# Kernel tuning notes

Measured on AMD Instinct MI355X. Metric: run time of the kernel, lower is better.

## Reference

```python
import jax, jax.numpy as jnp
import numpy as np

TOP_K = 2


def setup_inputs() -> dict:
    key = jax.random.key(0)
    k_x, k_g, k_w1, k_w2, k_w3 = jax.random.split(key, 5)
    B, S, D, H, E = 2, 512, 1024, 512, 8
    x = jax.random.normal(k_x, (B, S, D), dtype=jnp.float32)
    gate_w = jax.random.normal(k_g, (D, E), dtype=jnp.float32) * (D ** -0.5)
    w1 = jax.random.normal(k_w1, (E, D, H), dtype=jnp.float32) * 0.02  # gate proj
    w2 = jax.random.normal(k_w2, (E, H, D), dtype=jnp.float32) * 0.02  # down proj
    w3 = jax.random.normal(k_w3, (E, D, H), dtype=jnp.float32) * 0.02  # up proj
    return {"x": x, "gate_w": gate_w, "w1": w1, "w2": w2, "w3": w3}


def reference(x, gate_w, w1, w2, w3):
    # Token-choice top-k MoE with grouped SwiGLU experts, no shared expert.
    # Equivalent to torchtune MoE: gather routed tokens, scale by top-k router
    # score, run per-expert FFN, scatter-add back. Since each expert's FFN has
    # no bias (FFN(0) == 0), the dispatch/grouped-GEMM/combine is expressed
    # densely as sum_e FFN_e(scale[:, e] * x), which is mathematically identical.
    B, S, D = x.shape
    E = gate_w.shape[1]
    xf = x.reshape(B * S, D)                      # [T, D]
    T = B * S

    logits = xf @ gate_w                          # [T, E]
    scores = jax.nn.softmax(logits, axis=-1)
    top_scores, top_idx = jax.lax.top_k(scores, TOP_K)  # [T, k]

    # scale[t, e] = router score if expert e selected for token t, else 0
    scale = jnp.zeros((T, E), dtype=x.dtype).at[
        jnp.arange(T)[:, None], top_idx
    ].set(top_scores)

    xs = scale.T[:, :, None] * xf[None, :, :]     # [E, T, D] scaled routed input
    h = jax.nn.silu(jnp.einsum('etd,edh->eth', xs, w1)) \
        * jnp.einsum('etd,edh->eth', xs, w3)      # [E, T, H]
    y = jnp.einsum('eth,ehd->etd', h, w2)         # [E, T, D]
    out = y.sum(axis=0)                           # combine (scatter-add equiv)
    return out.reshape(B, S, D)
```

## Files before the change

### kernel.cpp

```cpp
#include <hip/hip_runtime.h>
#include <hip/hip_bf16.h>
#include <cstddef>

#define T_TOK 1024
#define D_DIM 1024
#define H_DIM 512
#define E_EXP 8
#define P_CAP 2560
#define MAX_MT 40
#define LDA 72
#define NK1 16
#define NK2 8

typedef __attribute__((ext_vector_type(4)))  float    float4_t;
typedef __attribute__((ext_vector_type(16))) float    f32x16;
typedef __attribute__((ext_vector_type(8)))  short    short8_t;
typedef __attribute__((ext_vector_type(4)))  unsigned uint4_t;
typedef __attribute__((ext_vector_type(2)))  unsigned uint2_t;

__device__ __forceinline__ short f2bf(float f) {
  union { float f; unsigned u; } v; v.f = f;
  unsigned u = v.u;
  u += 0x7FFFu + ((u >> 16) & 1u);
  return (short)(u >> 16);
}

__device__ __forceinline__ unsigned pkbf(float a, float b) {
  union { __hip_bfloat162 h; unsigned u; } v;
  v.h = __float22bfloat162_rn(make_float2(a, b));
  return v.u;
}

__global__ __launch_bounds__(256) void prep_kernel(
    const float* __restrict__ w1, const float* __restrict__ w3,
    const float* __restrict__ w2, const float* __restrict__ x,
    const float* __restrict__ gw, short* __restrict__ w13t,
    short* __restrict__ w2t, int* __restrict__ idx2,
    float* __restrict__ scale2, float* __restrict__ out) {
  __shared__ float tile[64][69];
  const int z = blockIdx.z;
  const int tid = threadIdx.x;

  if (z < 24) {
    const float* src; short* dst; int N, ldd, row_off;
    if (z < 16) {
      if (blockIdx.y >= 8) return;
      int which = z >> 3, e = z & 7;
      src = (which ? w3 : w1) + (size_t)e * D_DIM * H_DIM;
      dst = w13t + (size_t)e * D_DIM * (2 * H_DIM);
      N = H_DIM; ldd = D_DIM; row_off = which ? H_DIM : 0;
    } else {
      if (blockIdx.x >= 8) return;
      int e = z - 16;
      src = w2 + (size_t)e * H_DIM * D_DIM;
      dst = w2t + (size_t)e * D_DIM * H_DIM;
      N = D_DIM; ldd = H_DIM; row_off = 0;
    }
    const int k0 = blockIdx.x * 64, n0 = blockIdx.y * 64;
    const int kr = tid >> 4, nc = (tid & 15) * 4;
    #pragma unroll
    for (int p = 0; p < 4; ++p) {
      int k = p * 16 + kr;
      float4_t v = *(const float4_t*)(src + (size_t)(k0 + k) * N + n0 + nc);
      tile[k][nc]     = v[0];
      tile[k][nc + 1] = v[1];
      tile[k][nc + 2] = v[2];
      tile[k][nc + 3] = v[3];
    }
    __syncthreads();
    const int r8 = tid >> 3, c8 = tid & 7;
    #pragma unroll
    for (int p = 0; p < 2; ++p) {
      int row = p * 32 + r8;
      uint4_t u;
      #pragma unroll
      for (int jj = 0; jj < 4; ++jj)
        u[jj] = pkbf(tile[c8 * 8 + 2 * jj][row], tile[c8 * 8 + 2 * jj + 1][row]);
      *(uint4_t*)(dst + (size_t)(row_off + n0 + row) * ldd + k0 + c8 * 8) = u;
    }
    return;
  }

  if (z == 25) {
    float4_t z4 = {0.f, 0.f, 0.f, 0.f};
    float4_t* o = (float4_t*)(out + ((size_t)(blockIdx.y * 16 + blockIdx.x)) * 4096);
    #pragma unroll
    for (int i = 0; i < 4; ++i) o[i * 256 + tid] = z4;
    return;
  }

  const int wid  = tid >> 6;
  const int lane = tid & 63;
  const int t = (blockIdx.y * 16 + blockIdx.x) * 4 + wid;
  const float* xr = x + (size_t)t * D_DIM;
  float acc[E_EXP];
  #pragma unroll
  for (int e = 0; e < E_EXP; ++e) acc[e] = 0.f;
  for (int d = lane; d < D_DIM; d += 64) {
    float xv = xr[d];
    float4_t g0 = *(const float4_t*)(gw + d * E_EXP);
    float4_t g1 = *(const float4_t*)(gw + d * E_EXP + 4);
    acc[0] += xv * g0[0]; acc[1] += xv * g0[1];
    acc[2] += xv * g0[2]; acc[3] += xv * g0[3];
    acc[4] += xv * g1[0]; acc[5] += xv * g1[1];
    acc[6] += xv * g1[2]; acc[7] += xv * g1[3];
  }
  #pragma unroll
  for (int off = 32; off >= 1; off >>= 1) {
    #pragma unroll
    for (int e = 0; e < E_EXP; ++e) acc[e] += __shfl_down(acc[e], off, 64);
  }
  if (lane == 0) {
    float m = acc[0];
    #pragma unroll
    for (int e = 1; e < E_EXP; ++e) m = fmaxf(m, acc[e]);
    float p[E_EXP]; float s = 0.f;
    #pragma unroll
    for (int e = 0; e < E_EXP; ++e) { p[e] = __expf(acc[e] - m); s += p[e]; }
    float inv = 1.f / s;
    #pragma unroll
    for (int e = 0; e < E_EXP; ++e) p[e] *= inv;
    int i1 = 0;
    #pragma unroll
    for (int e = 1; e < E_EXP; ++e) if (p[e] > p[i1]) i1 = e;
    int i2 = (i1 == 0) ? 1 : 0;
    #pragma unroll
    for (int e = 0; e < E_EXP; ++e) {
      if (e == i1 || e == i2) continue;
      if (p[e] > p[i2]) i2 = e;
    }
    idx2[2 * t]     = i1;  scale2[2 * t]     = p[i1];
    idx2[2 * t + 1] = i2;  scale2[2 * t + 1] = p[i2];
  }
}

__global__ __launch_bounds__(256) void scan_kernel(
    const int* __restrict__ idx2, const float* __restrict__ scale2,
    int* __restrict__ pair_tok, float* __restrict__ pair_scale,
    int* __restrict__ meta) {
  __shared__ int cnt[E_EXP], base[E_EXP], cur[E_EXP];
  const int tid = threadIdx.x;
  if (tid < E_EXP) { cnt[tid] = 0; cur[tid] = 0; }
  for (int p = tid; p < P_CAP; p += 256) { pair_tok[p] = -1; pair_scale[p] = 0.f; }
  __syncthreads();
  for (int t = tid; t < T_TOK; t += 256) {
    atomicAdd(&cnt[idx2[2 * t]], 1);
    atomicAdd(&cnt[idx2[2 * t + 1]], 1);
  }
  __syncthreads();
  if (tid == 0) {
    int b = 0, g = 0;
    for (int e = 0; e < E_EXP; ++e) {
      base[e] = b;
      int al = (cnt[e] + 63) & ~63;
      for (int j = 0; j < al; j += 64) { meta[1 + g] = e; meta[81 + g] = b + j; ++g; }
      b += al;
    }
    meta[0] = g;
  }
  __syncthreads();
  for (int t = tid; t < T_TOK; t += 256) {
    #pragma unroll
    for (int s = 0; s < 2; ++s) {
      int e = idx2[2 * t + s];
      int p = base[e] + atomicAdd(&cur[e], 1);
      pair_tok[p] = t;
      pair_scale[p] = scale2[2 * t + s];
    }
  }
}

__global__ __launch_bounds__(256) void astage_kernel(
    const float* __restrict__ x, const int* __restrict__ pair_tok,
    const float* __restrict__ pair_scale, short* __restrict__ Ag) {
  const int tid = threadIdx.x;
  const int row = blockIdx.x * 8 + (tid >> 5);
  const int c0  = (tid & 31) * 4;
  const int   tok = pair_tok[row];
  const float sc  = pair_scale[row];
  const float* xr = x + (size_t)(tok < 0 ? 0 : tok) * D_DIM;
  short* orow = Ag + (size_t)row * D_DIM;
  #pragma unroll
  for (int j = 0; j < 8; ++j) {
    int c = c0 + j * 128;
    float4_t v = *(const float4_t*)(xr + c);
    uint2_t u = { pkbf(v[0] * sc, v[1] * sc), pkbf(v[2] * sc, v[3] * sc) };
    *(uint2_t*)(orow + c) = u;
  }
}

__global__ __launch_bounds__(256, 2) void gemm1_kernel(
    const short* __restrict__ Ag, const short* __restrict__ w13t,
    const int* __restrict__ meta, short* __restrict__ h) {
  __shared__ short As[2][64 * LDA];
  __shared__ short B1s[2][64 * LDA];
  __shared__ short B3s[2][64 * LDA];
  const int mt = blockIdx.y;
  if (mt >= meta[0]) return;
  const int e    = meta[1 + mt];
  const int row0 = meta[81 + mt];
  const int n0   = blockIdx.x * 64;
  const int tid = threadIdx.x, lane = tid & 63, wid = tid >> 6;
  const int wm = wid >> 1, wn = wid & 1;
  const int l31 = lane & 31, lh = lane >> 5;
  const short* bsrc = w13t + (size_t)e * D_DIM * (2 * H_DIM);

  const int sr = tid >> 3, su = (tid & 7) * 8;
  const size_t st32 = (size_t)32 * D_DIM;
  const short* apA = Ag   + (size_t)(row0 + sr) * D_DIM + su;
  const short* ap1 = bsrc + (size_t)(n0 + sr) * D_DIM + su;
  const short* ap3 = bsrc + (size_t)(H_DIM + n0 + sr) * D_DIM + su;

  f32x16 acc1, acc3;
  #pragma unroll
  for (int i = 0; i < 16; ++i) { acc1[i] = 0.f; acc3[i] = 0.f; }

  {
    uint4_t a0 = *(const uint4_t*)apA;
    uint4_t a1 = *(const uint4_t*)(apA + st32);
    uint4_t p0 = *(const uint4_t*)ap1;
    uint4_t p1 = *(const uint4_t*)(ap1 + st32);
    uint4_t q0 = *(const uint4_t*)ap3;
    uint4_t q1 = *(const uint4_t*)(ap3 + st32);
    *(uint4_t*)&As[0][sr * LDA + su]         = a0;
    *(uint4_t*)&As[0][(sr + 32) * LDA + su]  = a1;
    *(uint4_t*)&B1s[0][sr * LDA + su]        = p0;
    *(uint4_t*)&B1s[0][(sr + 32) * LDA + su] = p1;
    *(uint4_t*)&B3s[0][sr * LDA + su]        = q0;
    *(uint4_t*)&B3s[0][(sr + 32) * LDA + su] = q1;
  }

  for (int t = 0; t < NK1 - 1; ++t) {
    __syncthreads();
    const int cur = t & 1, nxt = cur ^ 1;
    const int ko = (t + 1) * 64;
    uint4_t a0 = *(const uint4_t*)(apA + ko);
    uint4_t a1 = *(const uint4_t*)(apA + st32 + ko);
    uint4_t p0 = *(const uint4_t*)(ap1 + ko);
    uint4_t p1 = *(const uint4_t*)(ap1 + st32 + ko);
    uint4_t q0 = *(const uint4_t*)(ap3 + ko);
    uint4_t q1 = *(const uint4_t*)(ap3 + st32 + ko);

    short8_t af[4], b1f[4], b3f[4];
    #pragma unroll
    for (int s = 0; s < 4; ++s) {
      const int kof = s * 16 + lh * 8;
      af[s]  = *(const short8_t*)&As[cur][(wm * 32 + l31) * LDA + kof];
      b1f[s] = *(const short8_t*)&B1s[cur][(wn * 32 + l31) * LDA + kof];
      b3f[s] = *(const short8_t*)&B3s[cur][(wn * 32 + l31) * LDA + kof];
    }
    #pragma unroll
    for (int s = 0; s < 4; ++s) {
      acc1 = __builtin_amdgcn_mfma_f32_32x32x16_bf16(af[s], b1f[s], acc1, 0, 0, 0);
      acc3 = __builtin_amdgcn_mfma_f32_32x32x16_bf16(af[s], b3f[s], acc3, 0, 0, 0);
    }
    *(uint4_t*)&As[nxt][sr * LDA + su]         = a0;
    *(uint4_t*)&As[nxt][(sr + 32) * LDA + su]  = a1;
    *(uint4_t*)&B1s[nxt][sr * LDA + su]        = p0;
    *(uint4_t*)&B1s[nxt][(sr + 32) * LDA + su] = p1;
    *(uint4_t*)&B3s[nxt][sr * LDA + su]        = q0;
    *(uint4_t*)&B3s[nxt][(sr + 32) * LDA + su] = q1;
  }
  __syncthreads();
  {
    short8_t af[4], b1f[4], b3f[4];
    #pragma unroll
    for (int s = 0; s < 4; ++s) {
      const int kof = s * 16 + lh * 8;
      af[s]  = *(const short8_t*)&As[1][(wm * 32 + l31) * LDA + kof];
      b1f[s] = *(const short8_t*)&B1s[1][(wn * 32 + l31) * LDA + kof];
      b3f[s] = *(const short8_t*)&B3s[1][(wn * 32 + l31) * LDA + kof];
    }
    #pragma unroll
    for (int s = 0; s < 4; ++s) {
      acc1 = __builtin_amdgcn_mfma_f32_32x32x16_bf16(af[s], b1f[s], acc1, 0, 0, 0);
      acc3 = __builtin_amdgcn_mfma_f32_32x32x16_bf16(af[s], b3f[s], acc3, 0, 0, 0);
    }
  }

  {
    const int col = n0 + wn * 32 + l31;
    #pragma unroll
    for (int r = 0; r < 16; ++r) {
      int mrow = (r & 3) + 8 * (r >> 2) + 4 * lh;
      int grow = row0 + wm * 32 + mrow;
      float c1 = acc1[r], c3 = acc3[r];
      float sig = 1.f / (1.f + __expf(-c1));
      h[(size_t)grow * H_DIM + col] = f2bf(c1 * sig * c3);
    }
  }
}

__global__ __launch_bounds__(256, 2) void gemm2_kernel(
    const short* __restrict__ h, const short* __restrict__ w2t,
    const int* __restrict__ pair_tok, const int* __restrict__ meta,
    float* __restrict__ out) {
  __shared__ short As[2][64 * LDA];
  __shared__ short Bs[2][128 * LDA];
  const int mt = blockIdx.y;
  if (mt >= meta[0]) return;
  const int e    = meta[1 + mt];
  const int row0 = meta[81 + mt];
  const int n0   = blockIdx.x * 128;
  const int tid = threadIdx.x, lane = tid & 63, wid = tid >> 6;
  const int wm = wid >> 1, wn = wid & 1;
  const int l31 = lane & 31, lh = lane >> 5;
  const short* bsrc = w2t + (size_t)e * D_DIM * H_DIM;

  const int sr = tid >> 3, su = (tid & 7) * 8;
  const size_t st32 = (size_t)32 * H_DIM;
  const short* apA = h    + (size_t)(row0 + sr) * H_DIM + su;
  const short* apB = bsrc + (size_t)(n0 + sr) * H_DIM + su;

  f32x16 acc[2];
  #pragma unroll
  for (int i = 0; i < 16; ++i) { acc[0][i] = 0.f; acc[1][i] = 0.f; }

  {
    uint4_t a0 = *(const uint4_t*)apA;
    uint4_t a1 = *(const uint4_t*)(apA + st32);
    uint4_t b0 = *(const uint4_t*)apB;
    uint4_t b1 = *(const uint4_t*)(apB + st32);
    uint4_t b2 = *(const uint4_t*)(apB + 2 * st32);
    uint4_t b3 = *(const uint4_t*)(apB + 3 * st32);
    *(uint4_t*)&As[0][sr * LDA + su]         = a0;
    *(uint4_t*)&As[0][(sr + 32) * LDA + su]  = a1;
    *(uint4_t*)&Bs[0][sr * LDA + su]         = b0;
    *(uint4_t*)&Bs[0][(sr + 32) * LDA + su]  = b1;
    *(uint4_t*)&Bs[0][(sr + 64) * LDA + su]  = b2;
    *(uint4_t*)&Bs[0][(sr + 96) * LDA + su]  = b3;
  }

  for (int t = 0; t < NK2 - 1; ++t) {
    __syncthreads();
    const int cur = t & 1, nxt = cur ^ 1;
    const int ko = (t + 1) * 64;
    uint4_t a0 = *(const uint4_t*)(apA + ko);
    uint4_t a1 = *(const uint4_t*)(apA + st32 + ko);
    uint4_t b0 = *(const uint4_t*)(apB + ko);
    uint4_t b1 = *(const uint4_t*)(apB + st32 + ko);
    uint4_t b2 = *(const uint4_t*)(apB + 2 * st32 + ko);
    uint4_t b3 = *(const uint4_t*)(apB + 3 * st32 + ko);

    short8_t af[4], bf[2][4];
    #pragma unroll
    for (int s = 0; s < 4; ++s) {
      const int kof = s * 16 + lh * 8;
      af[s] = *(const short8_t*)&As[cur][(wm * 32 + l31) * LDA + kof];
      #pragma unroll
      for (int j = 0; j < 2; ++j)
        bf[j][s] = *(const short8_t*)&Bs[cur][(wn * 64 + j * 32 + l31) * LDA + kof];
    }
    #pragma unroll
    for (int s = 0; s < 4; ++s) {
      acc[0] = __builtin_amdgcn_mfma_f32_32x32x16_bf16(af[s], bf[0][s], acc[0], 0, 0, 0);
      acc[1] = __builtin_amdgcn_mfma_f32_32x32x16_bf16(af[s], bf[1][s], acc[1], 0, 0, 0);
    }
    *(uint4_t*)&As[nxt][sr * LDA + su]         = a0;
    *(uint4_t*)&As[nxt][(sr + 32) * LDA + su]  = a1;
    *(uint4_t*)&Bs[nxt][sr * LDA + su]         = b0;
    *(uint4_t*)&Bs[nxt][(sr + 32) * LDA + su]  = b1;
    *(uint4_t*)&Bs[nxt][(sr + 64) * LDA + su]  = b2;
    *(uint4_t*)&Bs[nxt][(sr + 96) * LDA + su]  = b3;
  }
  __syncthreads();
  {
    short8_t af[4], bf[2][4];
    #pragma unroll
    for (int s = 0; s < 4; ++s) {
      const int kof = s * 16 + lh * 8;
      af[s] = *(const short8_t*)&As[1][(wm * 32 + l31) * LDA + kof];
      #pragma unroll
      for (int j = 0; j < 2; ++j)
        bf[j][s] = *(const short8_t*)&Bs[1][(wn * 64 + j * 32 + l31) * LDA + kof];
    }
    #pragma unroll
    for (int s = 0; s < 4; ++s) {
      acc[0] = __builtin_amdgcn_mfma_f32_32x32x16_bf16(af[s], bf[0][s], acc[0], 0, 0, 0);
      acc[1] = __builtin_amdgcn_mfma_f32_32x32x16_bf16(af[s], bf[1][s], acc[1], 0, 0, 0);
    }
  }

  {
    #pragma unroll
    for (int r = 0; r < 16; ++r) {
      int mrow = (r & 3) + 8 * (r >> 2) + 4 * lh;
      int grow = row0 + wm * 32 + mrow;
      int tok = pair_tok[grow];
      if (tok < 0) continue;
      float* orow = out + (size_t)tok * D_DIM;
      #pragma unroll
      for (int j = 0; j < 2; ++j) {
        int col = n0 + wn * 64 + j * 32 + l31;
        atomicAdd(orow + col, acc[j][r]);
      }
    }
  }
}

extern "C" void kernel_launch(void* const* d_in, const int* in_sizes, int n_in,
                              void* d_out, int out_size, void* d_ws, size_t ws_size,
                              hipStream_t stream) {
  const float* x  = (const float*)d_in[0];
  const float* gw = (const float*)d_in[1];
  const float* w1 = (const float*)d_in[2];
  const float* w2 = (const float*)d_in[3];
  const float* w3 = (const float*)d_in[4];
  float* out = (float*)d_out;

  char* ws = (char*)d_ws;
  int*   idx2    = (int*)  (ws);
  float* scale2  = (float*)(ws + 8192);
  int*   ptok    = (int*)  (ws + 16384);
  float* pscale  = (float*)(ws + 32768);
  int*   meta    = (int*)  (ws + 49152);
  short* h       = (short*)(ws + (1u << 20));
  short* w13t    = (short*)(ws + (4u << 20));
  short* w2t     = (short*)(ws + (21u << 20));
  short* Ag      = (short*)(ws + (30u << 20));

  prep_kernel<<<dim3(16, 16, 26), dim3(256), 0, stream>>>(
      w1, w3, w2, x, gw, w13t, w2t, idx2, scale2, out);
  scan_kernel<<<dim3(1), dim3(256), 0, stream>>>(idx2, scale2, ptok, pscale, meta);
  astage_kernel<<<dim3(P_CAP / 8), dim3(256), 0, stream>>>(x, ptok, pscale, Ag);
  gemm1_kernel<<<dim3(H_DIM / 64, MAX_MT), dim3(256), 0, stream>>>(
      Ag, w13t, meta, h);
  gemm2_kernel<<<dim3(D_DIM / 128, MAX_MT), dim3(256), 0, stream>>>(
      h, w2t, ptok, meta, out);
}
```

Before: 148.5 us.

## Fuse MoE pipeline into one persistent cooperative kernel with grid syncs

Replaces five separate launches (prep/transpose, scan, A staging, gemm1, gemm2) with a single cooperative persistent kernel of 512 blocks. The blocks loop over work units and separate the stages with grid.sync(). The aim is to remove launch gaps and tail idle time between the small stages. The cost is grid-wide barriers, a single-block scan phase while every other block waits, and fixed-grid scheduling of the GEMM tiles. The old multi-kernel path is kept as a fallback if the cooperative launch fails.

Result: slower. 393.2 us (+164.9%).

```diff
diff --git a/kernel.cpp b/kernel.cpp
--- a/kernel.cpp
+++ b/kernel.cpp
@@ -1,6 +1,9 @@
 #include <hip/hip_runtime.h>
+#include <hip/hip_cooperative_groups.h>
 #include <hip/hip_bf16.h>
 #include <cstddef>
+
+namespace cg = cooperative_groups;
 
 #define T_TOK 1024
 #define D_DIM 1024
@@ -11,6 +14,7 @@
 #define LDA 72
 #define NK1 16
 #define NK2 8
+#define GRID_B 512
 
 typedef __attribute__((ext_vector_type(4)))  float    float4_t;
 typedef __attribute__((ext_vector_type(16))) float    f32x16;
@@ -29,6 +33,364 @@
   union { __hip_bfloat162 h; unsigned u; } v;
   v.h = __float22bfloat162_rn(make_float2(a, b));
   return v.u;
+}
+
+union SharedU {
+  float tt[64 * 69];
+  struct { short A[2][64 * LDA], B1[2][64 * LDA], B3[2][64 * LDA]; } g1;
+  struct { short A[2][64 * LDA], B[2][128 * LDA]; } g2;
+};
+
+__device__ __forceinline__ void transpose_tile(
+    const float* __restrict__ src, short* __restrict__ dst, int N, int ldd,
+    int row_off, int k0, int n0, int tid, float* tt) {
+  const int kr = tid >> 4, nc = (tid & 15) * 4;
+  #pragma unroll
+  for (int p = 0; p < 4; ++p) {
+    int k = p * 16 + kr;
+    float4_t v = *(const float4_t*)(src + (size_t)(k0 + k) * N + n0 + nc);
+    tt[k * 69 + nc]     = v[0];
+    tt[k * 69 + nc + 1] = v[1];
+    tt[k * 69 + nc + 2] = v[2];
+    tt[k * 69 + nc + 3] = v[3];
+  }
+  __syncthreads();
+  const int r8 = tid >> 3, c8 = tid & 7;
+  #pragma unroll
+  for (int p = 0; p < 2; ++p) {
+    int row = p * 32 + r8;
+    uint4_t u;
+    #pragma unroll
+    for (int jj = 0; jj < 4; ++jj)
+      u[jj] = pkbf(tt[(c8 * 8 + 2 * jj) * 69 + row], tt[(c8 * 8 + 2 * jj + 1) * 69 + row]);
+    *(uint4_t*)(dst + (size_t)(row_off + n0 + row) * ldd + k0 + c8 * 8) = u;
+  }
+  __syncthreads();
+}
+
+__device__ __forceinline__ void router4(
+    int u, const float* __restrict__ x, const float* __restrict__ gw,
+    int* __restrict__ idx2, float* __restrict__ scale2, int tid) {
+  const int wid = tid >> 6, lane = tid & 63;
+  const int t = u * 4 + wid;
+  const float* xr = x + (size_t)t * D_DIM;
+  float acc[E_EXP];
+  #pragma unroll
+  for (int e = 0; e < E_EXP; ++e) acc[e] = 0.f;
+  for (int d = lane; d < D_DIM; d += 64) {
+    float xv = xr[d];
+    float4_t g0 = *(const float4_t*)(gw + d * E_EXP);
+    float4_t g1 = *(const float4_t*)(gw + d * E_EXP + 4);
+    acc[0] += xv * g0[0]; acc[1] += xv * g0[1];
+    acc[2] += xv * g0[2]; acc[3] += xv * g0[3];
+    acc[4] += xv * g1[0]; acc[5] += xv * g1[1];
+    acc[6] += xv * g1[2]; acc[7] += xv * g1[3];
+  }
+  #pragma unroll
+  for (int off = 32; off >= 1; off >>= 1) {
+    #pragma unroll
+    for (int e = 0; e < E_EXP; ++e) acc[e] += __shfl_down(acc[e], off, 64);
+  }
+  if (lane == 0) {
+    float m = acc[0];
+    #pragma unroll
+    for (int e = 1; e < E_EXP; ++e) m = fmaxf(m, acc[e]);
+    float p[E_EXP]; float s = 0.f;
+    #pragma unroll
+    for (int e = 0; e < E_EXP; ++e) { p[e] = __expf(acc[e] - m); s += p[e]; }
+    float inv = 1.f / s;
+    #pragma unroll
+    for (int e = 0; e < E_EXP; ++e) p[e] *= inv;
+    int i1 = 0;
+    #pragma unroll
+    for (int e = 1; e < E_EXP; ++e) if (p[e] > p[i1]) i1 = e;
+    int i2 = (i1 == 0) ? 1 : 0;
+    #pragma unroll
+    for (int e = 0; e < E_EXP; ++e) {
+      if (e == i1 || e == i2) continue;
+      if (p[e] > p[i2]) i2 = e;
+    }
+    idx2[2 * t]     = i1;  scale2[2 * t]     = p[i1];
+    idx2[2 * t + 1] = i2;  scale2[2 * t + 1] = p[i2];
+  }
+}
+
+__global__ __launch_bounds__(256, 2) void moe_fused(
+    const float* __restrict__ x, const float* __restrict__ gw,
+    const float* __restrict__ w1, const float* __restrict__ w2,
+    const float* __restrict__ w3, short* __restrict__ w13t,
+    short* __restrict__ w2t, int* __restrict__ idx2,
+    float* __restrict__ scale2, int* __restrict__ ptok,
+    float* __restrict__ pscale, int* __restrict__ meta,
+    short* __restrict__ Ag, short* __restrict__ h,
+    float* __restrict__ out) {
+  cg::grid_group grid = cg::this_grid();
+  __shared__ SharedU sh;
+  __shared__ int s_cnt[E_EXP], s_base[E_EXP], s_cur[E_EXP];
+  const int tid = threadIdx.x;
+  const int bid = blockIdx.x;
+
+  for (int u = bid; u < 3594; u += GRID_B) {
+    if (u < 2048) {
+      int z = u >> 7, rem = u & 127;
+      int kt = rem & 15, nt = rem >> 4;
+      int which = z >> 3, e = z & 7;
+      const float* src = (which ? w3 : w1) + (size_t)e * D_DIM * H_DIM;
+      short* dst = w13t + (size_t)e * D_DIM * (2 * H_DIM);
+      transpose_tile(src, dst, H_DIM, D_DIM, which ? H_DIM : 0,
+                     kt * 64, nt * 64, tid, sh.tt);
+    } else if (u < 3072) {
+      int v = u - 2048;
+      int e = v >> 7, rem = v & 127;
+      int kt = rem & 7, nt = rem >> 3;
+      const float* src = w2 + (size_t)e * H_DIM * D_DIM;
+      short* dst = w2t + (size_t)e * D_DIM * H_DIM;
+      transpose_tile(src, dst, D_DIM, H_DIM, 0, kt * 64, nt * 64, tid, sh.tt);
+    } else if (u < 3328) {
+      router4(u - 3072, x, gw, idx2, scale2, tid);
+    } else if (u < 3584) {
+      int v = u - 3328;
+      float4_t z4 = {0.f, 0.f, 0.f, 0.f};
+      float4_t* o = (float4_t*)(out + (size_t)v * 4096);
+      #pragma unroll
+      for (int i = 0; i < 4; ++i) o[i * 256 + tid] = z4;
+    } else {
+      int p = (u - 3584) * 256 + tid;
+      if (p < P_CAP) { ptok[p] = -1; pscale[p] = 0.f; }
+    }
+  }
+  grid.sync();
+
+  if (bid == 0) {
+    if (tid < E_EXP) { s_cnt[tid] = 0; s_cur[tid] = 0; }
+    __syncthreads();
+    for (int t = tid; t < T_TOK; t += 256) {
+      atomicAdd(&s_cnt[idx2[2 * t]], 1);
+      atomicAdd(&s_cnt[idx2[2 * t + 1]], 1);
+    }
+    __syncthreads();
+    if (tid == 0) {
+      int b = 0, g = 0;
+      for (int e = 0; e < E_EXP; ++e) {
+        s_base[e] = b;
+        int al = (s_cnt[e] + 63) & ~63;
+        for (int j = 0; j < al; j += 64) { meta[1 + g] = e; meta[81 + g] = b + j; ++g; }
+        b += al;
+      }
+      meta[0] = g;
+    }
+    __syncthreads();
+    for (int t = tid; t < T_TOK; t += 256) {
+      #pragma unroll
+      for (int s = 0; s < 2; ++s) {
+        int e = idx2[2 * t + s];
+        int p = s_base[e] + atomicAdd(&s_cur[e], 1);
+        ptok[p] = t;
+        pscale[p] = scale2[2 * t + s];
+      }
+    }
+  }
+  grid.sync();
+
+  for (int u = bid; u < P_CAP / 8; u += GRID_B) {
+    const int row = u * 8 + (tid >> 5);
+    const int c0  = (tid & 31) * 4;
+    const int   tok = ptok[row];
+    const float sc  = pscale[row];
+    const float* xr = x + (size_t)(tok < 0 ? 0 : tok) * D_DIM;
+    short* orow = Ag + (size_t)row * D_DIM;
+    #pragma unroll
+    for (int j = 0; j < 8; ++j) {
+      int c = c0 + j * 128;
+      float4_t v = *(const float4_t*)(xr + c);
+      uint2_t uu = { pkbf(v[0] * sc, v[1] * sc), pkbf(v[2] * sc, v[3] * sc) };
+      *(uint2_t*)(orow + c) = uu;
+    }
+  }
+  const int nmt = meta[0];
+  grid.sync();
+
+  const int lane = tid & 63, wid = tid >> 6;
+  const int wm = wid >> 1, wn = wid & 1;
+  const int l31 = lane & 31, lh = lane >> 5;
+  const int sr = tid >> 3, su = (tid & 7) * 8;
+
+  for (int u = bid; u < 8 * nmt; u += GRID_B) {
+    const int nt = u & 7, mt = u >> 3;
+    const int e = meta[1 + mt], row0 = meta[81 + mt];
+    const int n0 = nt * 64;
+    const short* bsrc = w13t + (size_t)e * D_DIM * (2 * H_DIM);
+    const size_t st32 = (size_t)32 * D_DIM;
+    const short* apA = Ag   + (size_t)(row0 + sr) * D_DIM + su;
+    const short* ap1 = bsrc + (size_t)(n0 + sr) * D_DIM + su;
+    const short* ap3 = bsrc + (size_t)(H_DIM + n0 + sr) * D_DIM + su;
+
+    f32x16 acc1, acc3;
+    #pragma unroll
+    for (int i = 0; i < 16; ++i) { acc1[i] = 0.f; acc3[i] = 0.f; }
+
+    {
+      uint4_t a0 = *(const uint4_t*)apA;
+      uint4_t a1 = *(const uint4_t*)(apA + st32);
+      uint4_t p0 = *(const uint4_t*)ap1;
+      uint4_t p1 = *(const uint4_t*)(ap1 + st32);
+      uint4_t q0 = *(const uint4_t*)ap3;
+      uint4_t q1 = *(const uint4_t*)(ap3 + st32);
+      *(uint4_t*)&sh.g1.A[0][sr * LDA + su]         = a0;
+      *(uint4_t*)&sh.g1.A[0][(sr + 32) * LDA + su]  = a1;
+      *(uint4_t*)&sh.g1.B1[0][sr * LDA + su]        = p0;
+      *(uint4_t*)&sh.g1.B1[0][(sr + 32) * LDA + su] = p1;
+      *(uint4_t*)&sh.g1.B3[0][sr * LDA + su]        = q0;
+      *(uint4_t*)&sh.g1.B3[0][(sr + 32) * LDA + su] = q1;
+    }
+    for (int t = 0; t < NK1 - 1; ++t) {
+      __syncthreads();
+      const int cur = t & 1, nxt = cur ^ 1;
+      const int ko = (t + 1) * 64;
+      uint4_t a0 = *(const uint4_t*)(apA + ko);
+      uint4_t a1 = *(const uint4_t*)(apA + st32 + ko);
+      uint4_t p0 = *(const uint4_t*)(ap1 + ko);
+      uint4_t p1 = *(const uint4_t*)(ap1 + st32 + ko);
+      uint4_t q0 = *(const uint4_t*)(ap3 + ko);
+      uint4_t q1 = *(const uint4_t*)(ap3 + st32 + ko);
+      short8_t af[4], b1f[4], b3f[4];
+      #pragma unroll
+      for (int s = 0; s < 4; ++s) {
+        const int kof = s * 16 + lh * 8;
+        af[s]  = *(const short8_t*)&sh.g1.A[cur][(wm * 32 + l31) * LDA + kof];
+        b1f[s] = *(const short8_t*)&sh.g1.B1[cur][(wn * 32 + l31) * LDA + kof];
+        b3f[s] = *(const short8_t*)&sh.g1.B3[cur][(wn * 32 + l31) * LDA + kof];
+      }
+      #pragma unroll
+      for (int s = 0; s < 4; ++s) {
+        acc1 = __builtin_amdgcn_mfma_f32_32x32x16_bf16(af[s], b1f[s], acc1, 0, 0, 0);
+        acc3 = __builtin_amdgcn_mfma_f32_32x32x16_bf16(af[s], b3f[s], acc3, 0, 0, 0);
+      }
+      *(uint4_t*)&sh.g1.A[nxt][sr * LDA + su]         = a0;
+      *(uint4_t*)&sh.g1.A[nxt][(sr + 32) * LDA + su]  = a1;
+      *(uint4_t*)&sh.g1.B1[nxt][sr * LDA + su]        = p0;
+      *(uint4_t*)&sh.g1.B1[nxt][(sr + 32) * LDA + su] = p1;
+      *(uint4_t*)&sh.g1.B3[nxt][sr * LDA + su]        = q0;
+      *(uint4_t*)&sh.g1.B3[nxt][(sr + 32) * LDA + su] = q1;
+    }
+    __syncthreads();
+    {
+      short8_t af[4], b1f[4], b3f[4];
+      #pragma unroll
+      for (int s = 0; s < 4; ++s) {
+        const int kof = s * 16 + lh * 8;
+        af[s]  = *(const short8_t*)&sh.g1.A[1][(wm * 32 + l31) * LDA + kof];
+        b1f[s] = *(const short8_t*)&sh.g1.B1[1][(wn * 32 + l31) * LDA + kof];
+        b3f[s] = *(const short8_t*)&sh.g1.B3[1][(wn * 32 + l31) * LDA + kof];
+      }
+      #pragma unroll
+      for (int s = 0; s < 4; ++s) {
+        acc1 = __builtin_amdgcn_mfma_f32_32x32x16_bf16(af[s], b1f[s], acc1, 0, 0, 0);
+        acc3 = __builtin_amdgcn_mfma_f32_32x32x16_bf16(af[s], b3f[s], acc3, 0, 0, 0);
+      }
+    }
+    __syncthreads();
+    {
+      const int col = n0 + wn * 32 + l31;
+      #pragma unroll
+      for (int r = 0; r < 16; ++r) {
+        int mrow = (r & 3) + 8 * (r >> 2) + 4 * lh;
+        int grow = row0 + wm * 32 + mrow;
+        float c1 = acc1[r], c3 = acc3[r];
+        float sig = 1.f / (1.f + __expf(-c1));
+        h[(size_t)grow * H_DIM + col] = f2bf(c1 * sig * c3);
+      }
+    }
+  }
+  grid.sync();
+
+  for (int u = bid; u < 8 * nmt; u += GRID_B) {
+    const int nt = u & 7, mt = u >> 3;
+    const int e = meta[1 + mt], row0 = meta[81 + mt];
+    const int n0 = nt * 128;
+    const short* bsrc = w2t + (size_t)e * D_DIM * H_DIM;
+    const size_t st32 = (size_t)32 * H_DIM;
+    const short* apA = h    + (size_t)(row0 + sr) * H_DIM + su;
+    const short* apB = bsrc + (size_t)(n0 + sr) * H_DIM + su;
+
+    f32x16 accA, accB;
+    #pragma unroll
+    for (int i = 0; i < 16; ++i) { accA[i] = 0.f; accB[i] = 0.f; }
+
+    {
+      uint4_t a0 = *(const uint4_t*)apA;
+      uint4_t a1 = *(const uint4_t*)(apA + st32);
+      uint4_t b0 = *(const uint4_t*)apB;
+      uint4_t b1 = *(const uint4_t*)(apB + st32);
+      uint4_t b2 = *(const uint4_t*)(apB + 2 * st32);
+      uint4_t b3 = *(const uint4_t*)(apB + 3 * st32);
+      *(uint4_t*)&sh.g2.A[0][sr * LDA + su]        = a0;
+      *(uint4_t*)&sh.g2.A[0][(sr + 32) * LDA + su] = a1;
+      *(uint4_t*)&sh.g2.B[0][sr * LDA + su]        = b0;
+      *(uint4_t*)&sh.g2.B[0][(sr + 32) * LDA + su] = b1;
+      *(uint4_t*)&sh.g2.B[0][(sr + 64) * LDA + su] = b2;
+      *(uint4_t*)&sh.g2.B[0][(sr + 96) * LDA + su] = b3;
+    }
+    for (int t = 0; t < NK2 - 1; ++t) {
+      __syncthreads();
+      const int cur = t & 1, nxt = cur ^ 1;
+      const int ko = (t + 1) * 64;
+      uint4_t a0 = *(const uint4_t*)(apA + ko);
+      uint4_t a1 = *(const uint4_t*)(apA + st32 + ko);
+      uint4_t b0 = *(const uint4_t*)(apB + ko);
+      uint4_t b1 = *(const uint4_t*)(apB + st32 + ko);
+      uint4_t b2 = *(const uint4_t*)(apB + 2 * st32 + ko);
+      uint4_t b3 = *(const uint4_t*)(apB + 3 * st32 + ko);
+      short8_t af[4], bf0[4], bf1[4];
+      #pragma unroll
+      for (int s = 0; s < 4; ++s) {
+        const int kof = s * 16 + lh * 8;
+        af[s]  = *(const short8_t*)&sh.g2.A[cur][(wm * 32 + l31) * LDA + kof];
+        bf0[s] = *(const short8_t*)&sh.g2.B[cur][(wn * 64 + l31) * LDA + kof];
+        bf1[s] = *(const short8_t*)&sh.g2.B[cur][(wn * 64 + 32 + l31) * LDA + kof];
+      }
+      #pragma unroll
+      for (int s = 0; s < 4; ++s) {
+        accA = __builtin_amdgcn_mfma_f32_32x32x16_bf16(af[s], bf0[s], accA, 0, 0, 0);
+        accB = __builtin_amdgcn_mfma_f32_32x32x16_bf16(af[s], bf1[s], accB, 0, 0, 0);
+      }
+      *(uint4_t*)&sh.g2.A[nxt][sr * LDA + su]        = a0;
+      *(uint4_t*)&sh.g2.A[nxt][(sr + 32) * LDA + su] = a1;
+      *(uint4_t*)&sh.g2.B[nxt][sr * LDA + su]        = b0;
+      *(uint4_t*)&sh.g2.B[nxt][(sr + 32) * LDA + su] = b1;
+      *(uint4_t*)&sh.g2.B[nxt][(sr + 64) * LDA + su] = b2;
+      *(uint4_t*)&sh.g2.B[nxt][(sr + 96) * LDA + su] = b3;
+    }
+    __syncthreads();
+    {
+      short8_t af[4], bf0[4], bf1[4];
+      #pragma unroll
+      for (int s = 0; s < 4; ++s) {
+        const int kof = s * 16 + lh * 8;
+        af[s]  = *(const short8_t*)&sh.g2.A[1][(wm * 32 + l31) * LDA + kof];
+        bf0[s] = *(const short8_t*)&sh.g2.B[1][(wn * 64 + l31) * LDA + kof];
+        bf1[s] = *(const short8_t*)&sh.g2.B[1][(wn * 64 + 32 + l31) * LDA + kof];
+      }
+      #pragma unroll
+      for (int s = 0; s < 4; ++s) {
+        accA = __builtin_amdgcn_mfma_f32_32x32x16_bf16(af[s], bf0[s], accA, 0, 0, 0);
+        accB = __builtin_amdgcn_mfma_f32_32x32x16_bf16(af[s], bf1[s], accB, 0, 0, 0);
+      }
+    }
+    __syncthreads();
+    {
+      #pragma unroll
+      for (int r = 0; r < 16; ++r) {
+        int mrow = (r & 3) + 8 * (r >> 2) + 4 * lh;
+        int grow = row0 + wm * 32 + mrow;
+        int tok = ptok[grow];
+        if (tok < 0) continue;
+        float* orow = out + (size_t)tok * D_DIM;
+        atomicAdd(orow + n0 + wn * 64 + l31, accA[r]);
+        atomicAdd(orow + n0 + wn * 64 + 32 + l31, accB[r]);
+      }
+    }
+  }
 }
 
 __global__ __launch_bounds__(256) void prep_kernel(
@@ -37,12 +399,11 @@
     const float* __restrict__ gw, short* __restrict__ w13t,
     short* __restrict__ w2t, int* __restrict__ idx2,
     float* __restrict__ scale2, float* __restrict__ out) {
-  __shared__ float tile[64][69];
+  __shared__ float tile[64 * 69];
   const int z = blockIdx.z;
   const int tid = threadIdx.x;
-
   if (z < 24) {
-    const float* src; short* dst; int N, ldd, row_off;
+    const float* src; short* dst; int N, ldd, row_off, k0, n0;
     if (z < 16) {
       if (blockIdx.y >= 8) return;
       int which = z >> 3, e = z & 7;
@@ -56,31 +417,10 @@
       dst = w2t + (size_t)e * D_DIM * H_DIM;
       N = D_DIM; ldd = H_DIM; row_off = 0;
     }
-    const int k0 = blockIdx.x * 64, n0 = blockIdx.y * 64;
-    const int kr = tid >> 4, nc = (tid & 15) * 4;
-    #pragma unroll
-    for (int p = 0; p < 4; ++p) {
-      int k = p * 16 + kr;
-      float4_t v = *(const float4_t*)(src + (size_t)(k0 + k) * N + n0 + nc);
-      tile[k][nc]     = v[0];
-      tile[k][nc + 1] = v[1];
-      tile[k][nc + 2] = v[2];
-      tile[k][nc + 3] = v[3];
-    }
-    __syncthreads();
-    const int r8 = tid >> 3, c8 = tid & 7;
-    #pragma unroll
-    for (int p = 0; p < 2; ++p) {
-      int row = p * 32 + r8;
-      uint4_t u;
-      #pragma unroll
-      for (int jj = 0; jj < 4; ++jj)
-        u[jj] = pkbf(tile[c8 * 8 + 2 * jj][row], tile[c8 * 8 + 2 * jj + 1][row]);
-      *(uint4_t*)(dst + (size_t)(row_off + n0 + row) * ldd + k0 + c8 * 8) = u;
-    }
+    k0 = blockIdx.x * 64; n0 = blockIdx.y * 64;
+    transpose_tile(src, dst, N, ldd, row_off, k0, n0, tid, tile);
     return;
   }
-
   if (z == 25) {
     float4_t z4 = {0.f, 0.f, 0.f, 0.f};
     float4_t* o = (float4_t*)(out + ((size_t)(blockIdx.y * 16 + blockIdx.x)) * 4096);
@@ -88,50 +428,7 @@
     for (int i = 0; i < 4; ++i) o[i * 256 + tid] = z4;
     return;
   }
-
-  const int wid  = tid >> 6;
-  const int lane = tid & 63;
-  const int t = (blockIdx.y * 16 + blockIdx.x) * 4 + wid;
-  const float* xr = x + (size_t)t * D_DIM;
-  float acc[E_EXP];
-  #pragma unroll
-  for (int e = 0; e < E_EXP; ++e) acc[e] = 0.f;
-  for (int d = lane; d < D_DIM; d += 64) {
-    float xv = xr[d];
-    float4_t g0 = *(const float4_t*)(gw + d * E_EXP);
-    float4_t g1 = *(const float4_t*)(gw + d * E_EXP + 4);
-    acc[0] += xv * g0[0]; acc[1] += xv * g0[1];
-    acc[2] += xv * g0[2]; acc[3] += xv * g0[3];
-    acc[4] += xv * g1[0]; acc[5] += xv * g1[1];
-    acc[6] += xv * g1[2]; acc[7] += xv * g1[3];
-  }
-  #pragma unroll
-  for (int off = 32; off >= 1; off >>= 1) {
-    #pragma unroll
-    for (int e = 0; e < E_EXP; ++e) acc[e] += __shfl_down(acc[e], off, 64);
-  }
-  if (lane == 0) {
-    float m = acc[0];
-    #pragma unroll
-    for (int e = 1; e < E_EXP; ++e) m = fmaxf(m, acc[e]);
-    float p[E_EXP]; float s = 0.f;
-    #pragma unroll
-    for (int e = 0; e < E_EXP; ++e) { p[e] = __expf(acc[e] - m); s += p[e]; }
-    float inv = 1.f / s;
-    #pragma unroll
-    for (int e = 0; e < E_EXP; ++e) p[e] *= inv;
-    int i1 = 0;
-    #pragma unroll
-    for (int e = 1; e < E_EXP; ++e) if (p[e] > p[i1]) i1 = e;
-    int i2 = (i1 == 0) ? 1 : 0;
-    #pragma unroll
-    for (int e = 0; e < E_EXP; ++e) {
-      if (e == i1 || e == i2) continue;
-      if (p[e] > p[i2]) i2 = e;
-    }
-    idx2[2 * t]     = i1;  scale2[2 * t]     = p[i1];
-    idx2[2 * t + 1] = i2;  scale2[2 * t + 1] = p[i2];
-  }
+  router4(blockIdx.y * 16 + blockIdx.x, x, gw, idx2, scale2, tid);
 }
 
 __global__ __launch_bounds__(256) void scan_kernel(
@@ -192,44 +489,31 @@
 __global__ __launch_bounds__(256, 2) void gemm1_kernel(
     const short* __restrict__ Ag, const short* __restrict__ w13t,
     const int* __restrict__ meta, short* __restrict__ h) {
-  __shared__ short As[2][64 * LDA];
-  __shared__ short B1s[2][64 * LDA];
-  __shared__ short B3s[2][64 * LDA];
+  __shared__ SharedU sh;
   const int mt = blockIdx.y;
   if (mt >= meta[0]) return;
-  const int e    = meta[1 + mt];
-  const int row0 = meta[81 + mt];
-  const int n0   = blockIdx.x * 64;
+  const int e = meta[1 + mt], row0 = meta[81 + mt];
+  const int n0 = blockIdx.x * 64;
   const int tid = threadIdx.x, lane = tid & 63, wid = tid >> 6;
   const int wm = wid >> 1, wn = wid & 1;
   const int l31 = lane & 31, lh = lane >> 5;
+  const int sr = tid >> 3, su = (tid & 7) * 8;
   const short* bsrc = w13t + (size_t)e * D_DIM * (2 * H_DIM);
-
-  const int sr = tid >> 3, su = (tid & 7) * 8;
   const size_t st32 = (size_t)32 * D_DIM;
   const short* apA = Ag   + (size_t)(row0 + sr) * D_DIM + su;
   const short* ap1 = bsrc + (size_t)(n0 + sr) * D_DIM + su;
   const short* ap3 = bsrc + (size_t)(H_DIM + n0 + sr) * D_DIM + su;
-
   f32x16 acc1, acc3;
   #pragma unroll
   for (int i = 0; i < 16; ++i) { acc1[i] = 0.f; acc3[i] = 0.f; }
-
   {
-    uint4_t a0 = *(const uint4_t*)apA;
-    uint4_t a1 = *(const uint4_t*)(apA + st32);
-    uint4_t p0 = *(const uint4_t*)ap1;
-    uint4_t p1 = *(const uint4_t*)(ap1 + st32);
-    uint4_t q0 = *(const uint4_t*)ap3;
-    uint4_t q1 = *(const uint4_t*)(ap3 + st32);
-    *(uint4_t*)&As[0][sr * LDA + su]         = a0;
-    *(uint4_t*)&As[0][(sr + 32) * LDA + su]  = a1;
-    *(uint4_t*)&B1s[0][sr * LDA + su]        = p0;
-    *(uint4_t*)&B1s[0][(sr + 32) * LDA + su] = p1;
-    *(uint4_t*)&B3s[0][sr * LDA + su]        = q0;
-    *(uint4_t*)&B3s[0][(sr + 32) * LDA + su] = q1;
-  }
-
+    *(uint4_t*)&sh.g1.A[0][sr * LDA + su]         = *(const uint4_t*)apA;
+    *(uint4_t*)&sh.g1.A[0][(sr + 32) * LDA + su]  = *(const uint4_t*)(apA + st32);
+    *(uint4_t*)&sh.g1.B1[0][sr * LDA + su]        = *(const uint4_t*)ap1;
+    *(uint4_t*)&sh.g1.B1[0][(sr + 32) * LDA + su] = *(const uint4_t*)(ap1 + st32);
+    *(uint4_t*)&sh.g1.B3[0][sr * LDA + su]        = *(const uint4_t*)ap3;
+    *(uint4_t*)&sh.g1.B3[0][(sr + 32) * LDA + su] = *(const uint4_t*)(ap3 + st32);
+  }
   for (int t = 0; t < NK1 - 1; ++t) {
     __syncthreads();
     const int cur = t & 1, nxt = cur ^ 1;
@@ -240,26 +524,25 @@
     uint4_t p1 = *(const uint4_t*)(ap1 + st32 + ko);
     uint4_t q0 = *(const uint4_t*)(ap3 + ko);
     uint4_t q1 = *(const uint4_t*)(ap3 + st32 + ko);
-
     short8_t af[4], b1f[4], b3f[4];
     #pragma unroll
     for (int s = 0; s < 4; ++s) {
       const int kof = s * 16 + lh * 8;
-      af[s]  = *(const short8_t*)&As[cur][(wm * 32 + l31) * LDA + kof];
-      b1f[s] = *(const short8_t*)&B1s[cur][(wn * 32 + l31) * LDA + kof];
-      b3f[s] = *(const short8_t*)&B3s[cur][(wn * 32 + l31) * LDA + kof];
+      af[s]  = *(const short8_t*)&sh.g1.A[cur][(wm * 32 + l31) * LDA + kof];
+      b1f[s] = *(const short8_t*)&sh.g1.B1[cur][(wn * 32 + l31) * LDA + kof];
+      b3f[s] = *(const short8_t*)&sh.g1.B3[cur][(wn * 32 + l31) * LDA + kof];
     }
     #pragma unroll
     for (int s = 0; s < 4; ++s) {
       acc1 = __builtin_amdgcn_mfma_f32_32x32x16_bf16(af[s], b1f[s], acc1, 0, 0, 0);
       acc3 = __builtin_amdgcn_mfma_f32_32x32x16_bf16(af[s], b3f[s], acc3, 0, 0, 0);
     }
-    *(uint4_t*)&As[nxt][sr * LDA + su]         = a0;
-    *(uint4_t*)&As[nxt][(sr + 32) * LDA + su]  = a1;
-    *(uint4_t*)&B1s[nxt][sr * LDA + su]        = p0;
-    *(uint4_t*)&B1s[nxt][(sr + 32) * LDA + su] = p1;
-    *(uint4_t*)&B3s[nxt][sr * LDA + su]        = q0;
-    *(uint4_t*)&B3s[nxt][(sr + 32) * LDA + su] = q1;
+    *(uint4_t*)&sh.g1.A[nxt][sr * LDA + su]         = a0;
+    *(uint4_t*)&sh.g1.A[nxt][(sr + 32) * LDA + su]  = a1;
+    *(uint4_t*)&sh.g1.B1[nxt][sr * LDA + su]        = p0;
+    *(uint4_t*)&sh.g1.B1[nxt][(sr + 32) * LDA + su] = p1;
+    *(uint4_t*)&sh.g1.B3[nxt][sr * LDA + su]        = q0;
+    *(uint4_t*)&sh.g1.B3[nxt][(sr + 32) * LDA + su] = q1;
   }
   __syncthreads();
   {
@@ -267,9 +550,9 @@
     #pragma unroll
     for (int s = 0; s < 4; ++s) {
       const int kof = s * 16 + lh * 8;
-      af[s]  = *(const short8_t*)&As[1][(wm * 32 + l31) * LDA + kof];
-      b1f[s] = *(const short8_t*)&B1s[1][(wn * 32 + l31) * LDA + kof];
-      b3f[s] = *(const short8_t*)&B3s[1][(wn * 32 + l31) * LDA + kof];
+      af[s]  = *(const short8_t*)&sh.g1.A[1][(wm * 32 + l31) * LDA + kof];
+      b1f[s] = *(const short8_t*)&sh.g1.B1[1][(wn * 32 + l31) * LDA + kof];
+      b3f[s] = *(const short8_t*)&sh.g1.B3[1][(wn * 32 + l31) * LDA + kof];
     }
     #pragma unroll
     for (int s = 0; s < 4; ++s) {
@@ -277,7 +560,6 @@
       acc3 = __builtin_amdgcn_mfma_f32_32x32x16_bf16(af[s], b3f[s], acc3, 0, 0, 0);
     }
   }
-
   {
     const int col = n0 + wn * 32 + l31;
     #pragma unroll
@@ -295,42 +577,30 @@
     const short* __restrict__ h, const short* __restrict__ w2t,
     const int* __restrict__ pair_tok, const int* __restrict__ meta,
     float* __restrict__ out) {
-  __shared__ short As[2][64 * LDA];
-  __shared__ short Bs[2][128 * LDA];
+  __shared__ SharedU sh;
   const int mt = blockIdx.y;
   if (mt >= meta[0]) return;
-  const int e    = meta[1 + mt];
-  const int row0 = meta[81 + mt];
-  const int n0   = blockIdx.x * 128;
+  const int e = meta[1 + mt], row0 = meta[81 + mt];
+  const int n0 = blockIdx.x * 128;
   const int tid = threadIdx.x, lane = tid & 63, wid = tid >> 6;
   const int wm = wid >> 1, wn = wid & 1;
   const int l31 = lane & 31, lh = lane >> 5;
+  const int sr = tid >> 3, su = (tid & 7) * 8;
   const short* bsrc = w2t + (size_t)e * D_DIM * H_DIM;
-
-  const int sr = tid >> 3, su = (tid & 7) * 8;
   const size_t st32 = (size_t)32 * H_DIM;
   const short* apA = h    + (size_t)(row0 + sr) * H_DIM + su;
   const short* apB = bsrc + (size_t)(n0 + sr) * H_DIM + su;
-
-  f32x16 acc[2];
+  f32x16 accA, accB;
   #pragma unroll
-  for (int i = 0; i < 16; ++i) { acc[0][i] = 0.f; acc[1][i] = 0.f; }
-
+  for (int i = 0; i < 16; ++i) { accA[i] = 0.f; accB[i] = 0.f; }
   {
-    uint4_t a0 = *(const uint4_t*)apA;
-    uint4_t a1 = *(const uint4_t*)(apA + st32);
-    uint4_t b0 = *(const uint4_t*)apB;
-    uint4_t b1 = *(const uint4_t*)(apB + st32);
-    uint4_t b2 = *(const uint4_t*)(apB + 2 * st32);
-    uint4_t b3 = *(const uint4_t*)(apB + 3 * st32);
-    *(uint4_t*)&As[0][sr * LDA + su]         = a0;
-    *(uint4_t*)&As[0][(sr + 32) * LDA + su]  = a1;
-    *(uint4_t*)&Bs[0][sr * LDA + su]         = b0;
-    *(uint4_t*)&Bs[0][(sr + 32) * LDA + su]  = b1;
-    *(uint4_t*)&Bs[0][(sr + 64) * LDA + su]  = b2;
-    *(uint4_t*)&Bs[0][(sr + 96) * LDA + su]  = b3;
-  }
-
+    *(uint4_t*)&sh.g2.A[0][sr * LDA + su]        = *(const uint4_t*)apA;
+    *(uint4_t*)&sh.g2.A[0][(sr + 32) * LDA + su] = *(const uint4_t*)(apA + st32);
+    *(uint4_t*)&sh.g2.B[0][sr * LDA + su]        = *(const uint4_t*)apB;
+    *(uint4_t*)&sh.g2.B[0][(sr + 32) * LDA + su] = *(const uint4_t*)(apB + st32);
+    *(uint4_t*)&sh.g2.B[0][(sr + 64) * LDA + su] = *(const uint4_t*)(apB + 2 * st32);
+    *(uint4_t*)&sh.g2.B[0][(sr + 96) * LDA + su] = *(const uint4_t*)(apB + 3 * st32);
+  }
   for (int t = 0; t < NK2 - 1; ++t) {
     __syncthreads();
     const int cur = t & 1, nxt = cur ^ 1;
@@ -341,46 +611,42 @@
     uint4_t b1 = *(const uint4_t*)(apB + st32 + ko);
     uint4_t b2 = *(const uint4_t*)(apB + 2 * st32 + ko);
     uint4_t b3 = *(const uint4_t*)(apB + 3 * st32 + ko);
-
-    short8_t af[4], bf[2][4];
+    short8_t af[4], bf0[4], bf1[4];
     #pragma unroll
     for (int s = 0; s < 4; ++s) {
       const int kof = s * 16 + lh * 8;
-      af[s] = *(const short8_t*)&As[cur][(wm * 32 + l31) * LDA + kof];
-      #pragma unroll
-      for (int j = 0; j < 2; ++j)
-        bf[j][s] = *(const short8_t*)&Bs[cur][(wn * 64 + j * 32 + l31) * LDA + kof];
+      af[s]  = *(const short8_t*)&sh.g2.A[cur][(wm * 32 + l31) * LDA + kof];
+      bf0[s] = *(const short8_t*)&sh.g2.B[cur][(wn * 64 + l31) * LDA + kof];
+      bf1[s] = *(const short8_t*)&sh.g2.B[cur][(wn * 64 + 32 + l31) * LDA + kof];
     }
     #pragma unroll
     for (int s = 0; s < 4; ++s) {
-      acc[0] = __builtin_amdgcn_mfma_f32_32x32x16_bf16(af[s], bf[0][s], acc[0], 0, 0, 0);
-      acc[1] = __builtin_amdgcn_mfma_f32_32x32x16_bf16(af[s], bf[1][s], acc[1], 0, 0, 0);
-    }
-    *(uint4_t*)&As[nxt][sr * LDA + su]         = a0;
-    *(uint4_t*)&As[nxt][(sr + 32) * LDA + su]  = a1;
-    *(uint4_t*)&Bs[nxt][sr * LDA + su]         = b0;
-    *(uint4_t*)&Bs[nxt][(sr + 32) * LDA + su]  = b1;
-    *(uint4_t*)&Bs[nxt][(sr + 64) * LDA + su]  = b2;
-    *(uint4_t*)&Bs[nxt][(sr + 96) * LDA + su]  = b3;
+      accA = __builtin_amdgcn_mfma_f32_32x32x16_bf16(af[s], bf0[s], accA, 0, 0, 0);
+      accB = __builtin_amdgcn_mfma_f32_32x32x16_bf16(af[s], bf1[s], accB, 0, 0, 0);
+    }
+    *(uint4_t*)&sh.g2.A[nxt][sr * LDA + su]        = a0;
+    *(uint4_t*)&sh.g2.A[nxt][(sr + 32) * LDA + su] = a1;
+    *(uint4_t*)&sh.g2.B[nxt][sr * LDA + su]        = b0;
+    *(uint4_t*)&sh.g2.B[nxt][(sr + 32) * LDA + su] = b1;
+    *(uint4_t*)&sh.g2.B[nxt][(sr + 64) * LDA + su] = b2;
+    *(uint4_t*)&sh.g2.B[nxt][(sr + 96) * LDA + su] = b3;
   }
   __syncthreads();
   {
-    short8_t af[4], bf[2][4];
+    short8_t af[4], bf0[4], bf1[4];
     #pragma unroll
     for (int s = 0; s < 4; ++s) {
       const int kof = s * 16 + lh * 8;
-      af[s] = *(const short8_t*)&As[1][(wm * 32 + l31) * LDA + kof];
-      #pragma unroll
-      for (int j = 0; j < 2; ++j)
-        bf[j][s] = *(const short8_t*)&Bs[1][(wn * 64 + j * 32 + l31) * LDA + kof];
+      af[s]  = *(const short8_t*)&sh.g2.A[1][(wm * 32 + l31) * LDA + kof];
+      bf0[s] = *(const short8_t*)&sh.g2.B[1][(wn * 64 + l31) * LDA + kof];
+      bf1[s] = *(const short8_t*)&sh.g2.B[1][(wn * 64 + 32 + l31) * LDA + kof];
     }
     #pragma unroll
     for (int s = 0; s < 4; ++s) {
-      acc[0] = __builtin_amdgcn_mfma_f32_32x32x16_bf16(af[s], bf[0][s], acc[0], 0, 0, 0);
-      acc[1] = __builtin_amdgcn_mfma_f32_32x32x16_bf16(af[s], bf[1][s], acc[1], 0, 0, 0);
-    }
-  }
-
+      accA = __builtin_amdgcn_mfma_f32_32x32x16_bf16(af[s], bf0[s], accA, 0, 0, 0);
+      accB = __builtin_amdgcn_mfma_f32_32x32x16_bf16(af[s], bf1[s], accB, 0, 0, 0);
+    }
+  }
   {
     #pragma unroll
     for (int r = 0; r < 16; ++r) {
@@ -389,11 +655,8 @@
       int tok = pair_tok[grow];
       if (tok < 0) continue;
       float* orow = out + (size_t)tok * D_DIM;
-      #pragma unroll
-      for (int j = 0; j < 2; ++j) {
-        int col = n0 + wn * 64 + j * 32 + l31;
-        atomicAdd(orow + col, acc[j][r]);
-      }
+      atomicAdd(orow + n0 + wn * 64 + l31, accA[r]);
+      atomicAdd(orow + n0 + wn * 64 + 32 + l31, accB[r]);
     }
   }
 }
@@ -419,12 +682,20 @@
   short* w2t     = (short*)(ws + (21u << 20));
   short* Ag      = (short*)(ws + (30u << 20));
 
-  prep_kernel<<<dim3(16, 16, 26), dim3(256), 0, stream>>>(
-      w1, w3, w2, x, gw, w13t, w2t, idx2, scale2, out);
-  scan_kernel<<<dim3(1), dim3(256), 0, stream>>>(idx2, scale2, ptok, pscale, meta);
-  astage_kernel<<<dim3(P_CAP / 8), dim3(256), 0, stream>>>(x, ptok, pscale, Ag);
-  gemm1_kernel<<<dim3(H_DIM / 64, MAX_MT), dim3(256), 0, stream>>>(
-      Ag, w13t, meta, h);
-  gemm2_kernel<<<dim3(D_DIM / 128, MAX_MT), dim3(256), 0, stream>>>(
-      h, w2t, ptok, meta, out);
-}
+  void* kargs[] = {(void*)&x, (void*)&gw, (void*)&w1, (void*)&w2, (void*)&w3,
+                   (void*)&w13t, (void*)&w2t, (void*)&idx2, (void*)&scale2,
+                   (void*)&ptok, (void*)&pscale, (void*)&meta, (void*)&Ag,
+                   (void*)&h, (void*)&out};
+  hipError_t err = hipLaunchCooperativeKernel(
+      (const void*)moe_fused, dim3(GRID_B), dim3(256), kargs, 0, stream);
+  if (err != hipSuccess) {
+    prep_kernel<<<dim3(16, 16, 26), dim3(256), 0, stream>>>(
+        w1, w3, w2, x, gw, w13t, w2t, idx2, scale2, out);
+    scan_kernel<<<dim3(1), dim3(256), 0, stream>>>(idx2, scale2, ptok, pscale, meta);
+    astage_kernel<<<dim3(P_CAP / 8), dim3(256), 0, stream>>>(x, ptok, pscale, Ag);
+    gemm1_kernel<<<dim3(H_DIM / 64, MAX_MT), dim3(256), 0, stream>>>(
+        Ag, w13t, meta, h);
+    gemm2_kernel<<<dim3(D_DIM / 128, MAX_MT), dim3(256), 0, stream>>>(
+        h, w2t, ptok, meta, out);
+  }
+}
```
